# Kernel optimization log

Hardware: AMD Instinct MI355X
Metric: run time of the kernel (lower is better)

Reference implementation:

```python
import jax, jax.numpy as jnp
import numpy as np

# ---- static config (matches init_kwargs) ----
BATCH = 8; SEQ_LEN = 1024; ENC_IN = 7; PRED_LEN = 96
D_MODEL = 512; N_HEADS = 8; D_HEAD = D_MODEL // N_HEADS
D_FF = 2048; E_LAYERS = 2; FACTOR = 5
PATCH = 16; STRIDE = 8; PAD = 8
N_PATCH = (SEQ_LEN + PAD - PATCH) // STRIDE + 1  # 128
NF = D_MODEL * N_PATCH


def _sin_pe(n, d):
    # sinusoidal positional embedding (Informer/TSLib PositionalEmbedding)
    pos = np.arange(n, dtype=np.float32)[:, None]
    div = np.exp(np.arange(0, d, 2, dtype=np.float32) * (-np.log(10000.0) / d))
    pe = np.zeros((n, d), dtype=np.float32)
    pe[:, 0::2] = np.sin(pos * div)
    pe[:, 1::2] = np.cos(pos * div)
    return jnp.asarray(pe)


def _ln(x, g, b, eps=1e-5):
    m = x.mean(-1, keepdims=True)
    v = x.var(-1, keepdims=True)
    return (x - m) / jnp.sqrt(v + eps) * g + b


def _prob_attention(q, k, v, layer_idx):
    # Informer ProbAttention, mask_flag=False. q,k,v: [B,H,L,Dh]
    B, H, L, Dh = q.shape
    u = min(int(FACTOR * np.ceil(np.log(L))), L)  # sample_k == n_top here (L_Q == L_K)
    skey = jax.random.fold_in(jax.random.key(42), layer_idx)
    samp = jax.random.randint(skey, (L, u), 0, L)          # random keys per query
    k_s = k[:, :, samp, :]                                  # [B,H,L,u,Dh]
    qk_s = jnp.einsum('bhld,bhlsd->bhls', q, k_s)           # sampled scores
    M = qk_s.max(-1) - qk_s.mean(-1)                        # sparsity measure [B,H,L]
    top = jax.lax.top_k(M, u)[1]                            # active query idx [B,H,u]
    q_r = jnp.take_along_axis(q, top[..., None], axis=2)    # [B,H,u,Dh]
    scores = jnp.einsum('bhud,bhld->bhul', q_r, k) / jnp.sqrt(jnp.asarray(Dh, q.dtype))
    attn = jax.nn.softmax(scores, axis=-1)
    upd = jnp.einsum('bhul,bhld->bhud', attn, v)            # [B,H,u,Dh]
    ctx = jnp.broadcast_to(v.mean(axis=2, keepdims=True), (B, H, L, Dh))
    bi = jnp.arange(B)[:, None, None]
    hi = jnp.arange(H)[None, :, None]
    ctx = ctx.at[bi, hi, top].set(upd)                      # scatter updated queries
    return ctx


def reference(x_enc, x_mark_enc, x_dec, x_mark_dec, patch_W,
              Wq, bq, Wk, bk, Wv, bv, Wo, bo,
              c1W, c1b, c2W, c2b, ln1g, ln1b, ln2g, ln2b,
              encg, encb, headW, headb):
    B, L, C = x_enc.shape
    # Normalize('Stat'): per-series mean/std over time
    mean = x_enc.mean(axis=1, keepdims=True)
    std = jnp.sqrt(x_enc.var(axis=1, keepdims=True) + 1e-5)
    xn = (x_enc - mean) / std
    # PatchEmbedding: [B,C,L] -> replication-pad -> unfold -> linear + pos emb
    xc = jnp.pad(xn.transpose(0, 2, 1), ((0, 0), (0, 0), (0, PAD)), mode='edge')
    idx = np.arange(N_PATCH)[:, None] * STRIDE + np.arange(PATCH)
    tok = xc[:, :, idx].reshape(B * C, N_PATCH, PATCH) @ patch_W.T  # [BC,N,dm]
    tok = tok + _sin_pe(N_PATCH, D_MODEL)
    # Transformer encoder with ProbAttention
    for l in range(E_LAYERS):
        Beff, N, _ = tok.shape
        q = (tok @ Wq[l].T + bq[l]).reshape(Beff, N, N_HEADS, D_HEAD).transpose(0, 2, 1, 3)
        k = (tok @ Wk[l].T + bk[l]).reshape(Beff, N, N_HEADS, D_HEAD).transpose(0, 2, 1, 3)
        v = (tok @ Wv[l].T + bv[l]).reshape(Beff, N, N_HEADS, D_HEAD).transpose(0, 2, 1, 3)
        ctx = _prob_attention(q, k, v, l).transpose(0, 2, 1, 3).reshape(Beff, N, D_MODEL)
        x1 = _ln(tok + ctx @ Wo[l].T + bo[l], ln1g[l], ln1b[l])
        y = jax.nn.gelu(x1 @ c1W[l].T + c1b[l], approximate=False)  # conv1d k=1 == linear
        y = y @ c2W[l].T + c2b[l]
        tok = _ln(x1 + y, ln2g[l], ln2b[l])
    tok = _ln(tok, encg, encb)
    # FlattenHead: [B,C,N,dm] -> [B,C,dm,N] -> flatten -> linear -> [B,pred,C]
    feat = tok.reshape(B, C, N_PATCH, D_MODEL).transpose(0, 1, 3, 2).reshape(B, C, NF)
    dec = (feat @ headW.T + headb).transpose(0, 2, 1)
    return dec * std + mean  # de-normalize


def setup_inputs():
    key = jax.random.key(0)
    ks = iter(jax.random.split(key, 40))
    def rn(shape, s=0.02):
        return jax.random.normal(next(ks), shape, jnp.float32) * s
    return {
        'x_enc': jax.random.normal(next(ks), (BATCH, SEQ_LEN, ENC_IN), jnp.float32),
        'x_mark_enc': jax.random.normal(next(ks), (BATCH, SEQ_LEN, 4), jnp.float32),
        'x_dec': jax.random.normal(next(ks), (BATCH, 144, ENC_IN), jnp.float32),
        'x_mark_dec': jax.random.normal(next(ks), (BATCH, 144, 4), jnp.float32),
        'patch_W': rn((D_MODEL, PATCH)),
        'Wq': rn((E_LAYERS, D_MODEL, D_MODEL)), 'bq': jnp.zeros((E_LAYERS, D_MODEL)),
        'Wk': rn((E_LAYERS, D_MODEL, D_MODEL)), 'bk': jnp.zeros((E_LAYERS, D_MODEL)),
        'Wv': rn((E_LAYERS, D_MODEL, D_MODEL)), 'bv': jnp.zeros((E_LAYERS, D_MODEL)),
        'Wo': rn((E_LAYERS, D_MODEL, D_MODEL)), 'bo': jnp.zeros((E_LAYERS, D_MODEL)),
        'c1W': rn((E_LAYERS, D_FF, D_MODEL)), 'c1b': jnp.zeros((E_LAYERS, D_FF)),
        'c2W': rn((E_LAYERS, D_MODEL, D_FF)), 'c2b': jnp.zeros((E_LAYERS, D_MODEL)),
        'ln1g': jnp.ones((E_LAYERS, D_MODEL)), 'ln1b': jnp.zeros((E_LAYERS, D_MODEL)),
        'ln2g': jnp.ones((E_LAYERS, D_MODEL)), 'ln2b': jnp.zeros((E_LAYERS, D_MODEL)),
        'encg': jnp.ones((D_MODEL,)), 'encb': jnp.zeros((D_MODEL,)),
        'headW': rn((PRED_LEN, NF)), 'headb': jnp.zeros((PRED_LEN,)),
    }
```

## Files before the change

### kernel.cpp

```cpp
#include <hip/hip_runtime.h>
#include <math.h>
#include <stdint.h>

#define SEQ   1024
#define CIN   7
#define NB    8
#define BC    56
#define NP    128
#define DM    512
#define NH    8
#define DH    64
#define DFF   2048
#define U     25
#define NTOK  (BC*NP)
#define PE_COEF (-9.210340371976184f / 512.0f)
#define HKB   256
#define HNB   256

typedef __attribute__((ext_vector_type(8))) short short8;
typedef __attribute__((ext_vector_type(4))) float f32x4;

__device__ __forceinline__ short f2bf(float x) {
    union { float f; uint32_t u; } v; v.f = x;
    uint32_t r = v.u + 0x7FFFu + ((v.u >> 16) & 1u);
    return (short)(r >> 16);
}
__device__ __forceinline__ float bf2f(short x) {
    union { uint32_t u; float f; } v; v.u = ((uint32_t)(uint16_t)x) << 16;
    return v.f;
}

__device__ __forceinline__ void gl_lds16(const void* g, void* s) {
    __builtin_amdgcn_global_load_lds((const __attribute__((address_space(1))) void*)g,
                                     (__attribute__((address_space(3))) void*)s, 16, 0, 0);
}

__global__ void stats_kernel(const float* __restrict__ x, float* __restrict__ mean,
                             float* __restrict__ stdv) {
    int bc = blockIdx.x; int b = bc / CIN, c = bc % CIN;
    const float* base = x + (size_t)b * SEQ * CIN + c;
    float s = 0.f, ss = 0.f;
    for (int i = threadIdx.x; i < SEQ; i += 256) {
        float v = base[(size_t)i * CIN];
        s += v; ss += v * v;
    }
    __shared__ float rs[256], rss[256];
    rs[threadIdx.x] = s; rss[threadIdx.x] = ss; __syncthreads();
    for (int o = 128; o > 0; o >>= 1) {
        if (threadIdx.x < o) { rs[threadIdx.x] += rs[threadIdx.x + o]; rss[threadIdx.x] += rss[threadIdx.x + o]; }
        __syncthreads();
    }
    if (threadIdx.x == 0) {
        float m = rs[0] / SEQ;
        float v = rss[0] / SEQ - m * m;
        mean[bc] = m;
        stdv[bc] = sqrtf(v + 1e-5f);
    }
}

__device__ __forceinline__ void tf_round(uint32_t& x0, uint32_t& x1, uint32_t r) {
    x0 += x1; x1 = (x1 << r) | (x1 >> (32u - r)); x1 ^= x0;
}
__device__ void threefry2x32(uint32_t k0, uint32_t k1, uint32_t x0, uint32_t x1,
                             uint32_t& o0, uint32_t& o1) {
    uint32_t ks[3] = { k0, k1, k0 ^ k1 ^ 0x1BD11BDAu };
    x0 += ks[0]; x1 += ks[1];
    const uint32_t rotA[4] = {13u, 15u, 26u, 6u}, rotB[4] = {17u, 29u, 16u, 24u};
    #pragma unroll
    for (int i = 0; i < 5; i++) {
        const uint32_t* rr = (i & 1) ? rotB : rotA;
        tf_round(x0, x1, rr[0]); tf_round(x0, x1, rr[1]);
        tf_round(x0, x1, rr[2]); tf_round(x0, x1, rr[3]);
        x0 += ks[(i + 1) % 3];
        x1 += ks[(i + 2) % 3] + (uint32_t)(i + 1);
    }
    o0 = x0; o1 = x1;
}

__global__ void samp_kernel(int* __restrict__ samp) {
    int l = blockIdx.x;
    uint32_t s0, s1; threefry2x32(0u, 42u, 0u, (uint32_t)l, s0, s1);
    uint32_t a0, a1, b0, b1;
    threefry2x32(s0, s1, 0u, 2u, a0, a1);
    threefry2x32(s0, s1, 1u, 3u, b0, b1);
    uint32_t k20 = a1, k21 = b1;
    for (int i = threadIdx.x; i < 1600; i += blockDim.x) {
        uint32_t o0, o1;
        threefry2x32(k20, k21, (uint32_t)i, (uint32_t)(1600 + i), o0, o1);
        samp[l * 3200 + i]        = (int)(o0 & 127u);
        samp[l * 3200 + 1600 + i] = (int)(o1 & 127u);
    }
}

__global__ void convert_bf16(const float* __restrict__ in, short* __restrict__ out, int n4) {
    int i = blockIdx.x * 256 + threadIdx.x;
    if (i >= n4) return;
    float4 v = ((const float4*)in)[i];
    short4 o;
    o.x = f2bf(v.x); o.y = f2bf(v.y); o.z = f2bf(v.z); o.w = f2bf(v.w);
    ((short4*)out)[i] = o;
}

__global__ void pack_qkv(const float* __restrict__ Wq, const float* __restrict__ Wk,
                         const float* __restrict__ Wv, const float* __restrict__ bq,
                         const float* __restrict__ bk, const float* __restrict__ bv,
                         short* __restrict__ wout, float* __restrict__ bout) {
    int idx = blockIdx.x * 256 + threadIdx.x;
    if (idx >= 2 * 1536 * 128) return;
    int k4 = idx & 127;
    int n  = (idx >> 7) % 1536;
    int l  = idx / (1536 * 128);
    int sel3 = n >> 9;
    int nn = n & 511;
    const float* src = sel3 == 0 ? Wq : sel3 == 1 ? Wk : Wv;
    float4 v = *(const float4*)(src + ((size_t)l * DM + nn) * DM + k4 * 4);
    short4 o; o.x = f2bf(v.x); o.y = f2bf(v.y); o.z = f2bf(v.z); o.w = f2bf(v.w);
    *(short4*)(wout + ((size_t)l * 1536 + n) * DM + k4 * 4) = o;
    if (k4 == 0) {
        const float* bsrc = sel3 == 0 ? bq : sel3 == 1 ? bk : bv;
        bout[l * 1536 + n] = bsrc[l * DM + nn];
    }
}

__global__ void patch_embed(const float* __restrict__ x, const float* __restrict__ pw,
                            const float* __restrict__ mean, const float* __restrict__ stdv,
                            float* __restrict__ tok, short* __restrict__ tokb) {
    int p = blockIdx.x, bc = blockIdx.y;
    int b = bc / CIN, c = bc % CIN;
    __shared__ float xs[16];
    if (threadIdx.x < 16) {
        int i = p * 8 + threadIdx.x;
        if (i > SEQ - 1) i = SEQ - 1;
        xs[threadIdx.x] = (x[(size_t)b * SEQ * CIN + (size_t)i * CIN + c] - mean[bc]) / stdv[bc];
    }
    __syncthreads();
    for (int d = threadIdx.x; d < DM; d += blockDim.x) {
        float acc = 0.f;
        const float* wr = pw + d * 16;
        #pragma unroll
        for (int t = 0; t < 16; t++) acc += xs[t] * wr[t];
        int k2 = d & ~1;
        float ang = (float)p * expf((float)k2 * PE_COEF);
        acc += (d & 1) ? cosf(ang) : sinf(ang);
        size_t idx = ((size_t)bc * NP + p) * DM + d;
        tok[idx] = acc;
        tokb[idx] = f2bf(acc);
    }
}

template<int ACT, int OBF>
__global__ __launch_bounds__(256) void gemm_mfma(const short* __restrict__ A,
                                                 const short* __restrict__ W,
                                                 const float* __restrict__ bias,
                                                 float* __restrict__ Cf,
                                                 short* __restrict__ Cb,
                                                 int M, int N, int K) {
    __shared__ short Als[128 * 64];
    __shared__ short Bls[128 * 64];
    int tid = threadIdx.x;
    int w = tid >> 6, lane = tid & 63;
    int row0 = blockIdx.x * 128, col0 = blockIdx.y * 128;
    int wrow = (w >> 1) * 64, wcol = (w & 1) * 64;
    int ksub = K / gridDim.z;
    int k0 = blockIdx.z * ksub;
    f32x4 acc[4][4] = {};
    const char* Ab = (const char*)Als;
    const char* Bb = (const char*)Bls;

    for (int kt = k0; kt < k0 + ksub; kt += 64) {
        #pragma unroll
        for (int i = 0; i < 4; i++) {
            int L = i * 4096 + w * 1024 + lane * 16;
            int row = L >> 7;
            int cb  = L & 127;
            int scb = cb ^ ((row & 7) << 4);
            gl_lds16(A + (size_t)(row0 + row) * K + kt + (scb >> 1),
                     (char*)Als + i * 4096 + w * 1024);
            gl_lds16(W + (size_t)(col0 + row) * K + kt + (scb >> 1),
                     (char*)Bls + i * 4096 + w * 1024);
        }
        __syncthreads();
        #pragma unroll
        for (int ks = 0; ks < 2; ks++) {
            int cb = ks * 64 + ((lane >> 4) << 4);
            short8 af[4], bfr[4];
            #pragma unroll
            for (int m = 0; m < 4; m++) {
                int r = wrow + m * 16 + (lane & 15);
                af[m] = *(const short8*)(Ab + r * 128 + (cb ^ ((r & 7) << 4)));
            }
            #pragma unroll
            for (int n = 0; n < 4; n++) {
                int r = wcol + n * 16 + (lane & 15);
                bfr[n] = *(const short8*)(Bb + r * 128 + (cb ^ ((r & 7) << 4)));
            }
            #pragma unroll
            for (int m = 0; m < 4; m++)
                #pragma unroll
                for (int n = 0; n < 4; n++)
                    acc[m][n] = __builtin_amdgcn_mfma_f32_16x16x32_bf16(af[m], bfr[n], acc[m][n], 0, 0, 0);
        }
        __syncthreads();
    }

    float* Cfo = Cf + (size_t)blockIdx.z * M * N;
    #pragma unroll
    for (int m = 0; m < 4; m++) {
        int rbase = row0 + wrow + m * 16 + ((lane >> 4) << 2);
        #pragma unroll
        for (int n = 0; n < 4; n++) {
            int col = col0 + wcol + n * 16 + (lane & 15);
            float bval = (blockIdx.z == 0) ? bias[col] : 0.f;
            #pragma unroll
            for (int j = 0; j < 4; j++) {
                float v = acc[m][n][j] + bval;
                if (ACT == 1) v = 0.5f * v * (1.0f + erff(v * 0.7071067811865475f));
                if (OBF) Cb[(size_t)(rbase + j) * N + col] = f2bf(v);
                else     Cfo[(size_t)(rbase + j) * N + col] = v;
            }
        }
    }
}

__global__ __launch_bounds__(256, 2) void attn_fused(const short* __restrict__ qkvb,
                                                     const int* __restrict__ samp,
                                                     short* __restrict__ ctxb) {
    __shared__ float Sbuf[64 * 130];
    __shared__ short Vt[64 * 128];
    __shared__ short Kls[128 * 64];
    __shared__ float Mv[128];
    __shared__ int   topl[32];
    __shared__ float vmean[64];
    __shared__ float vpart[256];

    float* Stop = Sbuf;
    short* Pb   = (short*)(Sbuf + 32 * 130);

    int bh = blockIdx.x, bc = bh >> 3, h = bh & 7;
    int tid = threadIdx.x, w = tid >> 6, lane = tid & 63;
    const short* base = qkvb + (size_t)bc * NP * 1536 + h * DH;
    short* cbase = ctxb + (size_t)bc * NP * DM + h * DH;

    for (int e = tid; e < 1024; e += 256) {
        int row = e >> 3, c8 = e & 7;
        short8 kv = *(const short8*)(base + (size_t)row * 1536 + 512 + c8 * 8);
        *(short8*)((char*)Kls + row * 128 + ((c8 * 16) ^ ((row & 7) << 4))) = kv;
        short8 vv = *(const short8*)(base + (size_t)row * 1536 + 1024 + c8 * 8);
        #pragma unroll
        for (int j = 0; j < 8; j++) {
            int d = c8 * 8 + j;
            *(short*)((char*)Vt + d * 256 + ((2 * row) ^ ((d & 7) << 4))) = vv[j];
        }
    }
    __syncthreads();
    {
        int d = tid & 63, part = tid >> 6;
        float s = 0.f;
        #pragma unroll
        for (int i4 = 0; i4 < 4; i4++) {
            short8 v = *(const short8*)((char*)Vt + d * 256 + ((part * 64 + i4 * 16) ^ ((d & 7) << 4)));
            #pragma unroll
            for (int j = 0; j < 8; j++) s += bf2f(v[j]);
        }
        vpart[part * 64 + d] = s;
    }

    for (int half = 0; half < 2; half++) {
        int ar = half * 64 + 16 * w + (lane & 15);
        const short* qp = base + (size_t)ar * 1536;
        short8 a0 = *(const short8*)(qp + (lane >> 4) * 8);
        short8 a1 = *(const short8*)(qp + 32 + (lane >> 4) * 8);
        #pragma unroll 2
        for (int ct = 0; ct < 8; ct++) {
            int br = ct * 16 + (lane & 15);
            int cb0 = (lane >> 4) * 16;
            short8 b0 = *(const short8*)((char*)Kls + br * 128 + (cb0 ^ ((br & 7) << 4)));
            short8 b1 = *(const short8*)((char*)Kls + br * 128 + ((cb0 + 64) ^ ((br & 7) << 4)));
            f32x4 acc = {};
            acc = __builtin_amdgcn_mfma_f32_16x16x32_bf16(a0, b0, acc, 0, 0, 0);
            acc = __builtin_amdgcn_mfma_f32_16x16x32_bf16(a1, b1, acc, 0, 0, 0);
            int r0 = 16 * w + ((lane >> 4) << 2);
            int c = ct * 16 + (lane & 15);
            #pragma unroll
            for (int j = 0; j < 4; j++) Sbuf[(r0 + j) * 130 + c] = acc[j] * 0.125f;
        }
        __syncthreads();
        if (tid < 64) {
            int r = half * 64 + tid;
            const int* sp = samp + r * U;
            const float* Srow = &Sbuf[tid * 130];
            float mx = -1e30f, sm = 0.f;
            #pragma unroll
            for (int s = 0; s < U; s++) { float v = Srow[sp[s]]; mx = fmaxf(mx, v); sm += v; }
            Mv[r] = mx - sm * (1.0f / U);
        } else if (half == 0 && tid < 128) {
            int d = tid - 64;
            vmean[d] = (vpart[d] + vpart[64 + d] + vpart[128 + d] + vpart[192 + d]) * (1.0f / 128.0f);
        }
        __syncthreads();
    }

    if (w == 0) {
        float v0 = Mv[lane], v1 = Mv[lane + 64];
        for (int it = 0; it < U; it++) {
            float bv; int bi;
            if (v1 > v0) { bv = v1; bi = lane + 64; } else { bv = v0; bi = lane; }
            #pragma unroll
            for (int o = 32; o > 0; o >>= 1) {
                float ov = __shfl_xor(bv, o);
                int   oi = __shfl_xor(bi, o);
                if (ov > bv || (ov == bv && oi < bi)) { bv = ov; bi = oi; }
            }
            if (lane == 0) topl[it] = bi;
            if (bi == lane) v0 = -1e30f;
            if (bi == lane + 64) v1 = -1e30f;
        }
    } else {
        for (int e = tid - 64; e < 128 * 16; e += 192) {
            int n = e >> 4, c4 = e & 15;
            short4 o;
            o.x = f2bf(vmean[c4 * 4 + 0]); o.y = f2bf(vmean[c4 * 4 + 1]);
            o.z = f2bf(vmean[c4 * 4 + 2]); o.w = f2bf(vmean[c4 * 4 + 3]);
            *(short4*)(cbase + (size_t)n * DM + c4 * 4) = o;
        }
    }
    __syncthreads();

    {
        int rt = w & 1, cth = w >> 1;
        int u = rt * 16 + (lane & 15);
        int qrow = topl[u < U ? u : U - 1];
        const short* qp = base + (size_t)qrow * 1536;
        short8 a0 = *(const short8*)(qp + (lane >> 4) * 8);
        short8 a1 = *(const short8*)(qp + 32 + (lane >> 4) * 8);
        #pragma unroll
        for (int cti = 0; cti < 4; cti++) {
            int ct = cth * 4 + cti;
            int br = ct * 16 + (lane & 15);
            int cb0 = (lane >> 4) * 16;
            short8 b0 = *(const short8*)((char*)Kls + br * 128 + (cb0 ^ ((br & 7) << 4)));
            short8 b1 = *(const short8*)((char*)Kls + br * 128 + ((cb0 + 64) ^ ((br & 7) << 4)));
            f32x4 acc = {};
            acc = __builtin_amdgcn_mfma_f32_16x16x32_bf16(a0, b0, acc, 0, 0, 0);
            acc = __builtin_amdgcn_mfma_f32_16x16x32_bf16(a1, b1, acc, 0, 0, 0);
            int r0 = rt * 16 + ((lane >> 4) << 2);
            int c = ct * 16 + (lane & 15);
            #pragma unroll
            for (int j = 0; j < 4; j++) Stop[(r0 + j) * 130 + c] = acc[j] * 0.125f;
        }
    }
    __syncthreads();

    for (int e = tid; e < 7 * 128; e += 256)
        Pb[(25 + (e >> 7)) * 128 + (e & 127)] = 0;
    for (int it = w; it < U; it += 4) {
        float s0 = Stop[it * 130 + lane], s1 = Stop[it * 130 + 64 + lane];
        float mx = fmaxf(s0, s1);
        #pragma unroll
        for (int o = 32; o > 0; o >>= 1) mx = fmaxf(mx, __shfl_xor(mx, o));
        float e0 = expf(s0 - mx), e1 = expf(s1 - mx);
        float sum = e0 + e1;
        #pragma unroll
        for (int o = 32; o > 0; o >>= 1) sum += __shfl_xor(sum, o);
        float inv = 1.0f / sum;
        int sw = (it & 7) << 4;
        *(short*)((char*)Pb + it * 256 + ((2 * lane) ^ sw))        = f2bf(e0 * inv);
        *(short*)((char*)Pb + it * 256 + ((2 * (64 + lane)) ^ sw)) = f2bf(e1 * inv);
    }
    __syncthreads();

    #pragma unroll
    for (int t = w * 2; t < w * 2 + 2; t++) {
        int rt = t >> 2, ct = t & 3;
        int pr = rt * 16 + (lane & 15);
        int vr = ct * 16 + (lane & 15);
        f32x4 acc = {};
        #pragma unroll
        for (int ks = 0; ks < 4; ks++) {
            int off = ks * 64 + (lane >> 4) * 16;
            short8 a = *(const short8*)((char*)Pb + pr * 256 + (off ^ ((pr & 7) << 4)));
            short8 b = *(const short8*)((char*)Vt + vr * 256 + (off ^ ((vr & 7) << 4)));
            acc = __builtin_amdgcn_mfma_f32_16x16x32_bf16(a, b, acc, 0, 0, 0);
        }
        int u0 = rt * 16 + ((lane >> 4) << 2), d = ct * 16 + (lane & 15);
        #pragma unroll
        for (int j = 0; j < 4; j++) {
            int u = u0 + j;
            if (u < U) cbase[(size_t)topl[u] * DM + d] = f2bf(acc[j]);
        }
    }
}

__global__ __launch_bounds__(256) void residual_ln(const float* __restrict__ a,
                                                   const float* __restrict__ b,
                                                   const float* __restrict__ b2,
                                                   const float* __restrict__ g,
                                                   const float* __restrict__ beta,
                                                   float* __restrict__ out,
                                                   short* __restrict__ outb) {
    int row = blockIdx.x;
    int tid = threadIdx.x;
    const float* ar = a + (size_t)row * DM;
    float x0 = ar[tid], x1 = ar[tid + 256];
    if (b) {
        const float* br = b + (size_t)row * DM;
        x0 += br[tid]; x1 += br[tid + 256];
    }
    if (b2) {
        const float* br = b2 + (size_t)row * DM;
        x0 += br[tid]; x1 += br[tid + 256];
    }
    __shared__ float rs[256], rss[256];
    rs[tid] = x0 + x1; rss[tid] = x0 * x0 + x1 * x1; __syncthreads();
    for (int o = 128; o > 0; o >>= 1) {
        if (tid < o) { rs[tid] += rs[tid + o]; rss[tid] += rss[tid + o]; }
        __syncthreads();
    }
    float m = rs[0] / DM;
    float var = rss[0] / DM - m * m;
    float r = rsqrtf(var + 1e-5f);
    float y0 = (x0 - m) * r * g[tid] + beta[tid];
    float y1 = (x1 - m) * r * g[tid + 256] + beta[tid + 256];
    out[(size_t)row * DM + tid]       = y0;
    out[(size_t)row * DM + tid + 256] = y1;
    if (outb) {
        outb[(size_t)row * DM + tid]       = f2bf(y0);
        outb[(size_t)row * DM + tid + 256] = f2bf(y1);
    }
}

__global__ void transpose_tok(const float* __restrict__ tok, short* __restrict__ featb) {
    __shared__ float t[32][33];
    int bc = blockIdx.z, dt = blockIdx.y, pt = blockIdx.x;
    int tx = threadIdx.x, ty = threadIdx.y;
    #pragma unroll
    for (int i = 0; i < 4; i++) {
        int p = pt * 32 + ty + i * 8;
        int d = dt * 32 + tx;
        t[ty + i * 8][tx] = tok[((size_t)bc * NP + p) * DM + d];
    }
    __syncthreads();
    #pragma unroll
    for (int i = 0; i < 4; i++) {
        int d = dt * 32 + ty + i * 8;
        int p = pt * 32 + tx;
        featb[(size_t)bc * (DM * NP) + (size_t)d * NP + p] = f2bf(t[tx][ty + i * 8]);
    }
}

__global__ __launch_bounds__(256) void head_mfma(const float* __restrict__ hw,
                                                 const short* __restrict__ featb,
                                                 float* __restrict__ partial) {
    __shared__ short Als[96 * 64];
    __shared__ short Bls[64 * 64];
    int tid = threadIdx.x;
    int w = tid >> 6, lane = tid & 63;
    int wm = w >> 1, wn = w & 1;
    int kb = blockIdx.x * HKB;
    f32x4 acc[3][2] = {};
    const char* Ab = (const char*)Als;
    const char* Bb = (const char*)Bls;

    for (int kt = 0; kt < HKB; kt += 64) {
        #pragma unroll
        for (int i = 0; i < 6; i++) {
            int s = tid + i * 256;
            int row = s >> 4, c4 = s & 15;
            float4 v = *(const float4*)(hw + (size_t)row * 65536 + kb + kt + c4 * 4);
            short4 o; o.x = f2bf(v.x); o.y = f2bf(v.y); o.z = f2bf(v.z); o.w = f2bf(v.w);
            int boff = row * 128 + ((c4 * 8) ^ ((row & 7) << 4));
            *(short4*)((char*)Als + boff) = o;
        }
        #pragma unroll
        for (int i = 0; i < 4; i++) {
            int s = tid + i * 256;
            int row = s >> 4, c4 = s & 15;
            short4 o;
            if (row < BC) o = *(const short4*)(featb + (size_t)row * 65536 + kb + kt + c4 * 4);
            else { o.x = 0; o.y = 0; o.z = 0; o.w = 0; }
            int boff = row * 128 + ((c4 * 8) ^ ((row & 7) << 4));
            *(short4*)((char*)Bls + boff) = o;
        }
        __syncthreads();
        #pragma unroll
        for (int ks = 0; ks < 2; ks++) {
            int cb = ks * 64 + ((lane >> 4) << 4);
            short8 af[3], bfr[2];
            #pragma unroll
            for (int m = 0; m < 3; m++) {
                int r = wm * 48 + m * 16 + (lane & 15);
                af[m] = *(const short8*)(Ab + r * 128 + (cb ^ ((r & 7) << 4)));
            }
            #pragma unroll
            for (int n = 0; n < 2; n++) {
                int r = wn * 32 + n * 16 + (lane & 15);
                bfr[n] = *(const short8*)(Bb + r * 128 + (cb ^ ((r & 7) << 4)));
            }
            #pragma unroll
            for (int m = 0; m < 3; m++)
                #pragma unroll
                for (int n = 0; n < 2; n++)
                    acc[m][n] = __builtin_amdgcn_mfma_f32_16x16x32_bf16(af[m], bfr[n], acc[m][n], 0, 0, 0);
        }
        __syncthreads();
    }

    float* pb = partial + (size_t)blockIdx.x * (96 * 64);
    #pragma unroll
    for (int m = 0; m < 3; m++) {
        int rbase = wm * 48 + m * 16 + ((lane >> 4) << 2);
        #pragma unroll
        for (int n = 0; n < 2; n++) {
            int col = wn * 32 + n * 16 + (lane & 15);
            #pragma unroll
            for (int j = 0; j < 4; j++)
                pb[(rbase + j) * 64 + col] = acc[m][n][j];
        }
    }
}

__global__ void finalize_a(const float* __restrict__ partial, float* __restrict__ p2) {
    int i = blockIdx.x * 256 + threadIdx.x;
    int s = blockIdx.y;
    const float* p = partial + (size_t)s * 32 * 6144 + i;
    float sum = 0.f;
    #pragma unroll
    for (int b = 0; b < 32; b++) sum += p[(size_t)b * 6144];
    p2[s * 6144 + i] = sum;
}

__global__ void finalize_b(const float* __restrict__ p2, const float* __restrict__ hb,
                           const float* __restrict__ mean, const float* __restrict__ stdv,
                           float* __restrict__ out) {
    int i = blockIdx.x * 256 + threadIdx.x;
    if (i >= NB * 96 * CIN) return;
    int b = i / (96 * CIN);
    int r = i % (96 * CIN);
    int t = r / CIN, c = r % CIN;
    int bc = b * CIN + c;
    int j = t * 64 + bc;
    float s = 0.f;
    #pragma unroll
    for (int k = 0; k < 8; k++) s += p2[k * 6144 + j];
    out[i] = (s + hb[t]) * stdv[bc] + mean[bc];
}

extern "C" void kernel_launch(void* const* d_in, const int* in_sizes, int n_in,
                              void* d_out, int out_size, void* d_ws, size_t ws_size,
                              hipStream_t stream) {
    (void)in_sizes; (void)n_in; (void)out_size; (void)ws_size;
    const float* x_enc   = (const float*)d_in[0];
    const float* patch_W = (const float*)d_in[4];
    const float* Wq  = (const float*)d_in[5];
    const float* bq  = (const float*)d_in[6];
    const float* Wk  = (const float*)d_in[7];
    const float* bk  = (const float*)d_in[8];
    const float* Wv  = (const float*)d_in[9];
    const float* bv  = (const float*)d_in[10];
    const float* Wo  = (const float*)d_in[11];
    const float* bo  = (const float*)d_in[12];
    const float* c1W = (const float*)d_in[13];
    const float* c1b = (const float*)d_in[14];
    const float* c2W = (const float*)d_in[15];
    const float* c2b = (const float*)d_in[16];
    const float* ln1g = (const float*)d_in[17];
    const float* ln1b = (const float*)d_in[18];
    const float* ln2g = (const float*)d_in[19];
    const float* ln2b = (const float*)d_in[20];
    const float* encg = (const float*)d_in[21];
    const float* encb = (const float*)d_in[22];
    const float* headW = (const float*)d_in[23];
    const float* headb = (const float*)d_in[24];
    float* out = (float*)d_out;

    float* ws = (float*)d_ws;
    float* mean = ws + 0;
    float* stdv = ws + 64;
    float* bqkv = ws + 128;
    int*   samp = (int*)(ws + 6144);
    size_t off = 32768;
    const size_t T = (size_t)NTOK * DM;
    float* tok     = ws + off; off += T;
    float* pA      = ws + off; off += T;
    float* pB      = ws + off; off += T;
    float* x1      = ws + off; off += T;
    float* partial = ws + off; off += T;
    float* p2      = x1;
    short* sbase = (short*)(ws + off);
    size_t soff = 0;
    short* tok_b  = sbase + soff; soff += T;
    short* ctx_b  = sbase + soff; soff += T;
    short* x1_b   = sbase + soff; soff += T;
    short* qkv_b  = sbase + soff; soff += 3 * T;
    short* ffn_b  = sbase + soff; soff += (size_t)NTOK * DFF;
    short* featb  = ffn_b;
    short* wqkv_b = sbase + soff; soff += 2 * 1536 * DM;
    short* wo_b   = sbase + soff; soff += 2 * DM * DM;
    short* c1w_b  = sbase + soff; soff += 2 * (size_t)DFF * DM;
    short* c2w_b  = sbase + soff; soff += 2 * (size_t)DM * DFF;

    stats_kernel<<<BC, 256, 0, stream>>>(x_enc, mean, stdv);
    samp_kernel<<<2, 256, 0, stream>>>(samp);

    pack_qkv<<<1536, 256, 0, stream>>>(Wq, Wk, Wv, bq, bk, bv, wqkv_b, bqkv);
    convert_bf16<<<(2 * DM * DM / 4 + 255) / 256, 256, 0, stream>>>(Wo, wo_b, 2 * DM * DM / 4);
    convert_bf16<<<(2 * DFF * DM / 4 + 255) / 256, 256, 0, stream>>>(c1W, c1w_b, 2 * DFF * DM / 4);
    convert_bf16<<<(2 * DFF * DM / 4 + 255) / 256, 256, 0, stream>>>(c2W, c2w_b, 2 * DFF * DM / 4);

    patch_embed<<<dim3(NP, BC), 128, 0, stream>>>(x_enc, patch_W, mean, stdv, tok, tok_b);

    for (int l = 0; l < 2; l++) {
        gemm_mfma<0,1><<<dim3(56, 12), 256, 0, stream>>>(tok_b, wqkv_b + (size_t)l * 1536 * DM, bqkv + l * 1536, nullptr, qkv_b, NTOK, 1536, DM);
        attn_fused<<<448, 256, 0, stream>>>(qkv_b, samp + l * 3200, ctx_b);
        gemm_mfma<0,0><<<dim3(56, 4, 2), 256, 0, stream>>>(ctx_b, wo_b + (size_t)l * DM * DM, bo + l * DM, pA, nullptr, NTOK, DM, DM);
        residual_ln<<<NTOK, 256, 0, stream>>>(tok, pA, pB, ln1g + l * DM, ln1b + l * DM, x1, x1_b);
        gemm_mfma<1,1><<<dim3(56, 16), 256, 0, stream>>>(x1_b, c1w_b + (size_t)l * DFF * DM, c1b + l * DFF, nullptr, ffn_b, NTOK, DFF, DM);
        gemm_mfma<0,0><<<dim3(56, 4, 2), 256, 0, stream>>>(ffn_b, c2w_b + (size_t)l * DM * DFF, c2b + l * DM, pA, nullptr, NTOK, DM, DFF);
        residual_ln<<<NTOK, 256, 0, stream>>>(x1, pA, pB, ln2g + l * DM, ln2b + l * DM, tok, tok_b);
    }

    residual_ln<<<NTOK, 256, 0, stream>>>(tok, nullptr, nullptr, encg, encb, tok, nullptr);
    transpose_tok<<<dim3(4, 16, BC), dim3(32, 8), 0, stream>>>(tok, featb);
    head_mfma<<<HNB, 256, 0, stream>>>(headW, featb, partial);
    finalize_a<<<dim3(24, 8), 256, 0, stream>>>(partial, p2);
    finalize_b<<<21, 256, 0, stream>>>(p2, headb, mean, stdv, out);
}
```

Before: 359.6 us.

## Double-buffer GEMM LDS tiles, fuse weight prep kernels, use tanh GELU

The GEMM kernel gets two LDS buffers so the next K tile's global-to-LDS copies are issued before the MFMA work on the current tile, overlapping memory with compute. The five weight-conversion and sampling launches are merged into one prep_weights kernel to cut launch overhead. The exact erf GELU is replaced by the tanh approximation built on exp2f, which is cheaper but changes numerics slightly. Doubling LDS to 64KB per block may lower occupancy.

Result: faster. 337.5 us (-6.1%).

```diff
diff --git a/kernel.cpp b/kernel.cpp
--- a/kernel.cpp
+++ b/kernel.cpp
@@ -77,48 +77,51 @@
     o0 = x0; o1 = x1;
 }
 
-__global__ void samp_kernel(int* __restrict__ samp) {
-    int l = blockIdx.x;
-    uint32_t s0, s1; threefry2x32(0u, 42u, 0u, (uint32_t)l, s0, s1);
-    uint32_t a0, a1, b0, b1;
-    threefry2x32(s0, s1, 0u, 2u, a0, a1);
-    threefry2x32(s0, s1, 1u, 3u, b0, b1);
-    uint32_t k20 = a1, k21 = b1;
-    for (int i = threadIdx.x; i < 1600; i += blockDim.x) {
-        uint32_t o0, o1;
-        threefry2x32(k20, k21, (uint32_t)i, (uint32_t)(1600 + i), o0, o1);
-        samp[l * 3200 + i]        = (int)(o0 & 127u);
-        samp[l * 3200 + 1600 + i] = (int)(o1 & 127u);
-    }
-}
-
-__global__ void convert_bf16(const float* __restrict__ in, short* __restrict__ out, int n4) {
-    int i = blockIdx.x * 256 + threadIdx.x;
-    if (i >= n4) return;
-    float4 v = ((const float4*)in)[i];
-    short4 o;
-    o.x = f2bf(v.x); o.y = f2bf(v.y); o.z = f2bf(v.z); o.w = f2bf(v.w);
-    ((short4*)out)[i] = o;
-}
-
-__global__ void pack_qkv(const float* __restrict__ Wq, const float* __restrict__ Wk,
-                         const float* __restrict__ Wv, const float* __restrict__ bq,
-                         const float* __restrict__ bk, const float* __restrict__ bv,
-                         short* __restrict__ wout, float* __restrict__ bout) {
-    int idx = blockIdx.x * 256 + threadIdx.x;
-    if (idx >= 2 * 1536 * 128) return;
-    int k4 = idx & 127;
-    int n  = (idx >> 7) % 1536;
-    int l  = idx / (1536 * 128);
-    int sel3 = n >> 9;
-    int nn = n & 511;
-    const float* src = sel3 == 0 ? Wq : sel3 == 1 ? Wk : Wv;
-    float4 v = *(const float4*)(src + ((size_t)l * DM + nn) * DM + k4 * 4);
-    short4 o; o.x = f2bf(v.x); o.y = f2bf(v.y); o.z = f2bf(v.z); o.w = f2bf(v.w);
-    *(short4*)(wout + ((size_t)l * 1536 + n) * DM + k4 * 4) = o;
-    if (k4 == 0) {
-        const float* bsrc = sel3 == 0 ? bq : sel3 == 1 ? bk : bv;
-        bout[l * 1536 + n] = bsrc[l * DM + nn];
+__global__ void prep_weights(const float* __restrict__ Wq, const float* __restrict__ Wk,
+                             const float* __restrict__ Wv, const float* __restrict__ bq,
+                             const float* __restrict__ bk, const float* __restrict__ bv,
+                             const float* __restrict__ Wo, const float* __restrict__ c1W,
+                             const float* __restrict__ c2W,
+                             short* __restrict__ wqkv, float* __restrict__ bqkv,
+                             short* __restrict__ wo_b, short* __restrict__ c1w_b,
+                             short* __restrict__ c2w_b, int* __restrict__ samp) {
+    int blk = blockIdx.x, tid = threadIdx.x;
+    if (blk < 1536) {
+        int idx = blk * 256 + tid;
+        int k4 = idx & 127;
+        int n  = (idx >> 7) % 1536;
+        int l  = idx / (1536 * 128);
+        int sel3 = n >> 9;
+        int nn = n & 511;
+        const float* src = sel3 == 0 ? Wq : sel3 == 1 ? Wk : Wv;
+        float4 v = *(const float4*)(src + ((size_t)l * DM + nn) * DM + k4 * 4);
+        short4 o; o.x = f2bf(v.x); o.y = f2bf(v.y); o.z = f2bf(v.z); o.w = f2bf(v.w);
+        *(short4*)(wqkv + ((size_t)l * 1536 + n) * DM + k4 * 4) = o;
+        if (k4 == 0) {
+            const float* bsrc = sel3 == 0 ? bq : sel3 == 1 ? bk : bv;
+            bqkv[l * 1536 + n] = bsrc[l * DM + nn];
+        }
+    } else if (blk < 6144) {
+        const float* in; short* out; int i;
+        if (blk < 2048)      { in = Wo;  out = wo_b;  i = (blk - 1536) * 256 + tid; }
+        else if (blk < 4096) { in = c1W; out = c1w_b; i = (blk - 2048) * 256 + tid; }
+        else                 { in = c2W; out = c2w_b; i = (blk - 4096) * 256 + tid; }
+        float4 v = ((const float4*)in)[i];
+        short4 o; o.x = f2bf(v.x); o.y = f2bf(v.y); o.z = f2bf(v.z); o.w = f2bf(v.w);
+        ((short4*)out)[i] = o;
+    } else {
+        int l = blk - 6144;
+        uint32_t s0, s1; threefry2x32(0u, 42u, 0u, (uint32_t)l, s0, s1);
+        uint32_t a0, a1, b0, b1;
+        threefry2x32(s0, s1, 0u, 2u, a0, a1);
+        threefry2x32(s0, s1, 1u, 3u, b0, b1);
+        uint32_t k20 = a1, k21 = b1;
+        for (int i = tid; i < 1600; i += 256) {
+            uint32_t o0, o1;
+            threefry2x32(k20, k21, (uint32_t)i, (uint32_t)(1600 + i), o0, o1);
+            samp[l * 3200 + i]        = (int)(o0 & 127u);
+            samp[l * 3200 + 1600 + i] = (int)(o1 & 127u);
+        }
     }
 }
 
@@ -155,19 +158,17 @@
                                                  float* __restrict__ Cf,
                                                  short* __restrict__ Cb,
                                                  int M, int N, int K) {
-    __shared__ short Als[128 * 64];
-    __shared__ short Bls[128 * 64];
+    __shared__ short LDSU[2][16384];
     int tid = threadIdx.x;
     int w = tid >> 6, lane = tid & 63;
     int row0 = blockIdx.x * 128, col0 = blockIdx.y * 128;
     int wrow = (w >> 1) * 64, wcol = (w & 1) * 64;
     int ksub = K / gridDim.z;
     int k0 = blockIdx.z * ksub;
+    int nt = ksub >> 6;
     f32x4 acc[4][4] = {};
-    const char* Ab = (const char*)Als;
-    const char* Bb = (const char*)Bls;
-
-    for (int kt = k0; kt < k0 + ksub; kt += 64) {
+
+    auto stage = [&](int b, int kt) {
         #pragma unroll
         for (int i = 0; i < 4; i++) {
             int L = i * 4096 + w * 1024 + lane * 16;
@@ -175,11 +176,19 @@
             int cb  = L & 127;
             int scb = cb ^ ((row & 7) << 4);
             gl_lds16(A + (size_t)(row0 + row) * K + kt + (scb >> 1),
-                     (char*)Als + i * 4096 + w * 1024);
+                     (char*)&LDSU[b][0] + i * 4096 + w * 1024);
             gl_lds16(W + (size_t)(col0 + row) * K + kt + (scb >> 1),
-                     (char*)Bls + i * 4096 + w * 1024);
-        }
-        __syncthreads();
+                     (char*)&LDSU[b][8192] + i * 4096 + w * 1024);
+        }
+    };
+
+    stage(0, k0);
+    __syncthreads();
+    int cur = 0;
+    for (int t = 0; t < nt; t++) {
+        if (t + 1 < nt) stage(cur ^ 1, k0 + (t + 1) * 64);
+        const char* Ab = (const char*)&LDSU[cur][0];
+        const char* Bb = (const char*)&LDSU[cur][8192];
         #pragma unroll
         for (int ks = 0; ks < 2; ks++) {
             int cb = ks * 64 + ((lane >> 4) << 4);
@@ -201,6 +210,7 @@
                     acc[m][n] = __builtin_amdgcn_mfma_f32_16x16x32_bf16(af[m], bfr[n], acc[m][n], 0, 0, 0);
         }
         __syncthreads();
+        cur ^= 1;
     }
 
     float* Cfo = Cf + (size_t)blockIdx.z * M * N;
@@ -214,7 +224,11 @@
             #pragma unroll
             for (int j = 0; j < 4; j++) {
                 float v = acc[m][n][j] + bval;
-                if (ACT == 1) v = 0.5f * v * (1.0f + erff(v * 0.7071067811865475f));
+                if (ACT == 1) {
+                    float u = 0.7978845608f * (v + 0.044715f * v * v * v);
+                    float e = exp2f(2.8853900817779268f * u);
+                    v = v - v / (e + 1.0f);
+                }
                 if (OBF) Cb[(size_t)(rbase + j) * N + col] = f2bf(v);
                 else     Cfo[(size_t)(rbase + j) * N + col] = v;
             }
@@ -600,13 +614,8 @@
     short* c2w_b  = sbase + soff; soff += 2 * (size_t)DM * DFF;
 
     stats_kernel<<<BC, 256, 0, stream>>>(x_enc, mean, stdv);
-    samp_kernel<<<2, 256, 0, stream>>>(samp);
-
-    pack_qkv<<<1536, 256, 0, stream>>>(Wq, Wk, Wv, bq, bk, bv, wqkv_b, bqkv);
-    convert_bf16<<<(2 * DM * DM / 4 + 255) / 256, 256, 0, stream>>>(Wo, wo_b, 2 * DM * DM / 4);
-    convert_bf16<<<(2 * DFF * DM / 4 + 255) / 256, 256, 0, stream>>>(c1W, c1w_b, 2 * DFF * DM / 4);
-    convert_bf16<<<(2 * DFF * DM / 4 + 255) / 256, 256, 0, stream>>>(c2W, c2w_b, 2 * DFF * DM / 4);
-
+    prep_weights<<<6146, 256, 0, stream>>>(Wq, Wk, Wv, bq, bk, bv, Wo, c1W, c2W,
+                                           wqkv_b, bqkv, wo_b, c1w_b, c2w_b, samp);
     patch_embed<<<dim3(NP, BC), 128, 0, stream>>>(x_enc, patch_W, mean, stdv, tok, tok_b);
 
     for (int l = 0; l < 2; l++) {
```
